# Kernel tuning notes

Hardware: AMD Instinct MI355X
Metric: run time of the kernel (lower is better)

The kernel has to match this reference:

```python
import jax, jax.numpy as jnp
import numpy as np

C = 128
EPS = 1e-5


def _ln(x, g, b):
    m = jnp.mean(x, axis=-1, keepdims=True)
    v = jnp.mean((x - m) ** 2, axis=-1, keepdims=True)
    return (x - m) * jax.lax.rsqrt(v + EPS) * g + b


def setup_inputs() -> dict:
    key = jax.random.key(0)
    ks = jax.random.split(key, 10)
    B, N = 1, 384
    s = 1.0 / np.sqrt(C)
    inp = {
        "z": jax.random.normal(ks[0], (B, N, N, C), dtype=jnp.float32),
        "ln1_g": jnp.ones((C,), jnp.float32),
        "ln1_b": jnp.zeros((C,), jnp.float32),
        "ln2_g": jnp.ones((C,), jnp.float32),
        "ln2_b": jnp.zeros((C,), jnp.float32),
        "Wa": jax.random.uniform(ks[1], (C, C), jnp.float32, -s, s),
        "ba": jnp.zeros((C,), jnp.float32),
        "Wga": jax.random.uniform(ks[2], (C, C), jnp.float32, -s, s),
        "bga": jnp.zeros((C,), jnp.float32),
        "Wb": jax.random.uniform(ks[3], (C, C), jnp.float32, -s, s),
        "bb": jnp.zeros((C,), jnp.float32),
        "Wgb": jax.random.uniform(ks[4], (C, C), jnp.float32, -s, s),
        "bgb": jnp.zeros((C,), jnp.float32),
        "Wg": jax.random.uniform(ks[5], (C, C), jnp.float32, -s, s),
        "bg": jnp.zeros((C,), jnp.float32),
        "Wo": jax.random.uniform(ks[6], (C, C), jnp.float32, -s, s),
        "bo": jnp.zeros((C,), jnp.float32),
    }
    return inp


def reference(z, ln1_g, ln1_b, ln2_g, ln2_b, Wa, ba, Wga, bga, Wb, bb, Wgb, bgb, Wg, bg, Wo, bo):
    # z: (B, i, j, c)
    zn = _ln(z, ln1_g, ln1_b)
    a = (zn @ Wa + ba) * jax.nn.sigmoid(zn @ Wga + bga)      # (B,i,k,c)
    b = (zn @ Wb + bb) * jax.nn.sigmoid(zn @ Wgb + bgb)      # (B,j,k,c)
    gate = jax.nn.sigmoid(zn @ Wg + bg)                      # (B,i,j,c)
    o = jnp.einsum('bikc,bjkc->bijc', a, b)                  # outgoing triangle update
    return gate * (_ln(o, ln2_g, ln2_b) @ Wo + bo)
```

## Files before the change

kernel.cpp:

```cpp
#include <hip/hip_runtime.h>
#include <stdint.h>

typedef _Float16 f16x8 __attribute__((ext_vector_type(8)));
typedef float floatx4 __attribute__((ext_vector_type(4)));

#define RR 147456
#define NC 128
#define NN 384

__device__ inline floatx4 zero4() { floatx4 v; v[0]=0.f; v[1]=0.f; v[2]=0.f; v[3]=0.f; return v; }
__device__ inline float sigmoidf_(float x) { return 1.f / (1.f + __expf(-x)); }

__global__ __launch_bounds__(256) void k0_wt(
    const float* __restrict__ w0, const float* __restrict__ w1,
    const float* __restrict__ w2, const float* __restrict__ w3,
    const float* __restrict__ w4, const float* __restrict__ w5,
    _Float16* __restrict__ wf)
{
  const float* w;
  switch (blockIdx.x) {
    case 0: w = w0; break; case 1: w = w1; break; case 2: w = w2; break;
    case 3: w = w3; break; case 4: w = w4; break; default: w = w5; break;
  }
  _Float16* out = wf + blockIdx.x * 16384;
  const int t = threadIdx.x;
  for (int it = 0; it < 64; ++it) {
    int f = it * 256 + t;
    int j  = f & 7;
    int ln = (f >> 3) & 63;
    int nt = (f >> 9) & 7;
    int k0 = f >> 12;
    int k = k0 * 32 + (ln >> 4) * 8 + j;
    int n = nt * 16 + (ln & 15);
    out[f] = (_Float16)w[k * 128 + n];
  }
}

__global__ __launch_bounds__(256, 4) void k2_ln_gemm(
    const float* __restrict__ z, const float* __restrict__ ln1g, const float* __restrict__ ln1b,
    const _Float16* __restrict__ wf,
    const float* __restrict__ ba, const float* __restrict__ bga,
    const float* __restrict__ bb, const float* __restrict__ bgb,
    const float* __restrict__ bg,
    _Float16* __restrict__ at, _Float16* __restrict__ bt, _Float16* __restrict__ gate)
{
  __shared__ __align__(16) _Float16 zns[64][136];
  __shared__ __align__(16) _Float16 bnc[4][32 * 72];
  const int t = threadIdx.x;
  const int w = t >> 6, lane = t & 63;
  const int l15 = lane & 15, quad = lane >> 4;
  const int r0 = blockIdx.x * 64;
  const int nt0 = w * 2;

  {
    const int g = lane >> 4, h = lane & 15;
    float4 ga = *(const float4*)(ln1g + h*8);
    float4 gb = *(const float4*)(ln1g + h*8 + 4);
    float4 bba = *(const float4*)(ln1b + h*8);
    float4 bbb = *(const float4*)(ln1b + h*8 + 4);
    #pragma unroll
    for (int rr = 0; rr < 4; ++rr) {
      int row = w * 16 + rr * 4 + g;
      const float* zp = z + (size_t)(r0 + row) * NC + h * 8;
      float4 xa = *(const float4*)zp;
      float4 xb = *(const float4*)(zp + 4);
      float s = xa.x + xa.y + xa.z + xa.w + xb.x + xb.y + xb.z + xb.w;
      float q = xa.x*xa.x + xa.y*xa.y + xa.z*xa.z + xa.w*xa.w
              + xb.x*xb.x + xb.y*xb.y + xb.z*xb.z + xb.w*xb.w;
      #pragma unroll
      for (int m = 1; m < 16; m <<= 1) { s += __shfl_xor(s, m); q += __shfl_xor(q, m); }
      float mean = s * (1.f/128.f);
      float var  = q * (1.f/128.f) - mean*mean;
      float rs = rsqrtf(var + 1e-5f);
      union { uint4 u; _Float16 hh[8]; } pk;
      pk.hh[0] = (_Float16)((xa.x - mean) * rs * ga.x + bba.x);
      pk.hh[1] = (_Float16)((xa.y - mean) * rs * ga.y + bba.y);
      pk.hh[2] = (_Float16)((xa.z - mean) * rs * ga.z + bba.z);
      pk.hh[3] = (_Float16)((xa.w - mean) * rs * ga.w + bba.w);
      pk.hh[4] = (_Float16)((xb.x - mean) * rs * gb.x + bbb.x);
      pk.hh[5] = (_Float16)((xb.y - mean) * rs * gb.y + bbb.y);
      pk.hh[6] = (_Float16)((xb.z - mean) * rs * gb.z + bbb.z);
      pk.hh[7] = (_Float16)((xb.w - mean) * rs * gb.w + bbb.w);
      *(uint4*)&zns[row][h * 8] = pk.u;
    }
  }
  __syncthreads();

  const _Float16* pw = wf + lane * 8;
  f16x8 bw[4][2];
  floatx4 acc[4][2];
  union PkU { unsigned int u; _Float16 h[2]; };
  PkU sig[4][2][2];

  auto loadw = [&](int slot) {
    const _Float16* p = pw + slot * 16384;
    #pragma unroll
    for (int k0 = 0; k0 < 4; ++k0)
      #pragma unroll
      for (int j = 0; j < 2; ++j)
        bw[k0][j] = *(const f16x8*)(p + (k0*8 + nt0 + j) * 512);
  };
  auto dogemm = [&]() {
    #pragma unroll
    for (int mt = 0; mt < 4; ++mt) {
      acc[mt][0] = zero4(); acc[mt][1] = zero4();
      #pragma unroll
      for (int k0 = 0; k0 < 4; ++k0) {
        f16x8 af = *(const f16x8*)&zns[mt*16 + l15][k0*32 + quad*8];
        acc[mt][0] = __builtin_amdgcn_mfma_f32_16x16x32_f16(af, bw[k0][0], acc[mt][0], 0, 0, 0);
        acc[mt][1] = __builtin_amdgcn_mfma_f32_16x16x32_f16(af, bw[k0][1], acc[mt][1], 0, 0, 0);
      }
    }
  };
  auto sigpack = [&](const float* big) {
    #pragma unroll
    for (int j = 0; j < 2; ++j) {
      float bgv = big[(nt0 + j)*16 + l15];
      #pragma unroll
      for (int mt = 0; mt < 4; ++mt) {
        sig[mt][j][0].h[0] = (_Float16)sigmoidf_(acc[mt][j][0] + bgv);
        sig[mt][j][0].h[1] = (_Float16)sigmoidf_(acc[mt][j][1] + bgv);
        sig[mt][j][1].h[0] = (_Float16)sigmoidf_(acc[mt][j][2] + bgv);
        sig[mt][j][1].h[1] = (_Float16)sigmoidf_(acc[mt][j][3] + bgv);
      }
    }
  };
  auto bounce_out = [&](_Float16* dst) {
    asm volatile("s_waitcnt lgkmcnt(0)" ::: "memory");
    _Float16* base = dst + (size_t)blockIdx.x * 8192 + w * 2048;
    #pragma unroll
    for (int i = 0; i < 4; ++i) {
      int f = i * 512 + lane * 8;
      int cp = f >> 6, pos = f & 63;
      uint4 v = *(const uint4*)&bnc[w][cp * 72 + pos];
      *(uint4*)(base + f) = v;
    }
  };
  auto combine_store = [&](const float* bia, _Float16* dst) {
    #pragma unroll
    for (int j = 0; j < 2; ++j) {
      int c = (nt0 + j)*16 + l15;
      float bav = bia[c];
      #pragma unroll
      for (int mt = 0; mt < 4; ++mt) {
        union { uint2 u2; _Float16 h[4]; } pk;
        pk.h[0] = (_Float16)((acc[mt][j][0] + bav) * (float)sig[mt][j][0].h[0]);
        pk.h[1] = (_Float16)((acc[mt][j][1] + bav) * (float)sig[mt][j][0].h[1]);
        pk.h[2] = (_Float16)((acc[mt][j][2] + bav) * (float)sig[mt][j][1].h[0]);
        pk.h[3] = (_Float16)((acc[mt][j][3] + bav) * (float)sig[mt][j][1].h[1]);
        *(uint2*)&bnc[w][(j*16 + l15) * 72 + mt*16 + quad*4] = pk.u2;
      }
    }
    bounce_out(dst);
  };

  loadw(1); dogemm(); sigpack(bga);
  loadw(0); dogemm();
  loadw(3);
  combine_store(ba, at);
  dogemm(); sigpack(bgb);
  loadw(2); dogemm();
  loadw(4);
  combine_store(bb, bt);
  dogemm();
  #pragma unroll
  for (int j = 0; j < 2; ++j) {
    float bgv = bg[(nt0 + j)*16 + l15];
    #pragma unroll
    for (int mt = 0; mt < 4; ++mt) {
      union { uint2 u2; _Float16 h[4]; } pk;
      #pragma unroll
      for (int r = 0; r < 4; ++r)
        pk.h[r] = (_Float16)sigmoidf_(acc[mt][j][r] + bgv);
      *(uint2*)&bnc[w][(j*16 + l15) * 72 + mt*16 + quad*4] = pk.u2;
    }
  }
  bounce_out(gate);
}

__global__ __launch_bounds__(256, 3) void k3_tri(
    const _Float16* __restrict__ at, const _Float16* __restrict__ bt, _Float16* __restrict__ o)
{
  __shared__ __align__(16) _Float16 As[2][128 * 40];
  __shared__ __align__(16) _Float16 Bs[2][128 * 40];
  const int t = threadIdx.x;
  const int w = t >> 6, lane = t & 63, l15 = lane & 15, quad = lane >> 4;
  const int c = blockIdx.y;
  const int i0 = (blockIdx.x / 3) * 128, j0 = (blockIdx.x % 3) * 128;
  const int wi = w >> 1, wj = w & 1;

  const int srow = t >> 1, sch = (t & 1) * 16;
  const _Float16* gaRow = at + (size_t)(i0 + srow) * 6 * 8192 + (size_t)c * 64;
  const _Float16* gbRow = bt + (size_t)(j0 + srow) * 6 * 8192 + (size_t)c * 64;
  _Float16* const pa0 = &As[0][srow * 40 + sch];
  _Float16* const pb0 = &Bs[0][srow * 40 + sch];
  _Float16* const pa1 = &As[1][srow * 40 + sch];
  _Float16* const pb1 = &Bs[1][srow * 40 + sch];

  floatx4 acc[4][4];
  #pragma unroll
  for (int mt = 0; mt < 4; ++mt)
    #pragma unroll
    for (int nt = 0; nt < 4; ++nt) acc[mt][nt] = zero4();

  f16x8 aP0,aP1,bP0,bP1, aQ0,aQ1,bQ0,bQ1;

  auto gofs = [&](int kk) -> size_t {
    int x = kk + sch;
    return (size_t)(x >> 6) * 8192 + (size_t)(x & 63);
  };
  auto gloadP = [&](int kk) {
    size_t go = gofs(kk);
    aP0 = *(const f16x8*)(gaRow + go); aP1 = *(const f16x8*)(gaRow + go + 8);
    bP0 = *(const f16x8*)(gbRow + go); bP1 = *(const f16x8*)(gbRow + go + 8);
  };
  auto gloadQ = [&](int kk) {
    size_t go = gofs(kk);
    aQ0 = *(const f16x8*)(gaRow + go); aQ1 = *(const f16x8*)(gaRow + go + 8);
    bQ0 = *(const f16x8*)(gbRow + go); bQ1 = *(const f16x8*)(gbRow + go + 8);
  };
  auto swriteP = [&](int buf) {
    _Float16* pa = buf ? pa1 : pa0; _Float16* pb = buf ? pb1 : pb0;
    *(f16x8*)pa = aP0; *(f16x8*)(pa + 8) = aP1;
    *(f16x8*)pb = bP0; *(f16x8*)(pb + 8) = bP1;
  };
  auto swriteQ = [&](int buf) {
    _Float16* pa = buf ? pa1 : pa0; _Float16* pb = buf ? pb1 : pb0;
    *(f16x8*)pa = aQ0; *(f16x8*)(pa + 8) = aQ1;
    *(f16x8*)pb = bQ0; *(f16x8*)(pb + 8) = bQ1;
  };
  auto compute = [&](int buf) {
    f16x8 af[4], bfr[4];
    #pragma unroll
    for (int mt = 0; mt < 4; ++mt)
      af[mt] = *(const f16x8*)&As[buf][(wi*64 + mt*16 + l15) * 40 + quad*8];
    #pragma unroll
    for (int nt = 0; nt < 4; ++nt)
      bfr[nt] = *(const f16x8*)&Bs[buf][(wj*64 + nt*16 + l15) * 40 + quad*8];
    #pragma unroll
    for (int mt = 0; mt < 4; ++mt)
      #pragma unroll
      for (int nt = 0; nt < 4; ++nt)
        acc[mt][nt] = __builtin_amdgcn_mfma_f32_16x16x32_f16(af[mt], bfr[nt], acc[mt][nt], 0, 0, 0);
  };

  gloadP(0); swriteP(0); gloadP(32);
  __syncthreads();
  #pragma unroll
  for (int s = 0; s < 12; s += 2) {
    if (s + 2 < 12) gloadQ((s + 2) * 32);
    compute(0);
    swriteP(1);
    __syncthreads();
    if (s + 3 < 12) gloadP((s + 3) * 32);
    compute(1);
    if (s + 2 < 12) { swriteQ(0); __syncthreads(); }
  }

  #pragma unroll
  for (int mt = 0; mt < 4; ++mt) {
    #pragma unroll
    for (int r = 0; r < 4; ++r) {
      int i = i0 + wi*64 + mt*16 + quad*4 + r;
      _Float16* obase = o + (size_t)(i*6 + (j0 >> 6) + wj) * 8192 + (size_t)c * 64;
      #pragma unroll
      for (int nt = 0; nt < 4; ++nt) obase[nt*16 + l15] = (_Float16)acc[mt][nt][r];
    }
  }
}

__global__ __launch_bounds__(256, 4) void k4_out(
    const _Float16* __restrict__ o, const _Float16* __restrict__ gate,
    const float* __restrict__ ln2g, const float* __restrict__ ln2b,
    const _Float16* __restrict__ wo5, const float* __restrict__ bo,
    float* __restrict__ out)
{
  __shared__ __align__(16) _Float16 osb[64][136];
  const int t = threadIdx.x;
  const int w = t >> 6, lane = t & 63, l15 = lane & 15, quad = lane >> 4;
  const int r0 = blockIdx.x * 64;
  const int nt0 = w * 2;

  {
    const _Float16* ob = o + (size_t)blockIdx.x * 8192;
    #pragma unroll
    for (int it = 0; it < 4; ++it) {
      int f = (it * 256 + t) * 8;
      int cx = f >> 6, p = f & 63;
      f16x8 v = *(const f16x8*)(ob + f);
      #pragma unroll
      for (int i = 0; i < 8; ++i) osb[p + i][cx] = v[i];
    }
  }
  __syncthreads();

  {
    const int g = lane >> 4, h = lane & 15;
    float4 ga = *(const float4*)(ln2g + h*8);
    float4 gb = *(const float4*)(ln2g + h*8 + 4);
    float4 bba = *(const float4*)(ln2b + h*8);
    float4 bbb = *(const float4*)(ln2b + h*8 + 4);
    #pragma unroll
    for (int rr = 0; rr < 4; ++rr) {
      int row = w * 16 + rr * 4 + g;
      f16x8 xv = *(const f16x8*)&osb[row][h*8];
      float x0 = (float)xv[0], x1 = (float)xv[1], x2 = (float)xv[2], x3 = (float)xv[3];
      float x4 = (float)xv[4], x5 = (float)xv[5], x6 = (float)xv[6], x7 = (float)xv[7];
      float s = x0+x1+x2+x3+x4+x5+x6+x7;
      float q = x0*x0+x1*x1+x2*x2+x3*x3+x4*x4+x5*x5+x6*x6+x7*x7;
      #pragma unroll
      for (int m = 1; m < 16; m <<= 1) { s += __shfl_xor(s, m); q += __shfl_xor(q, m); }
      float mean = s * (1.f/128.f);
      float var  = q * (1.f/128.f) - mean*mean;
      float rs = rsqrtf(var + 1e-5f);
      union { uint4 u; _Float16 hh[8]; } pk;
      pk.hh[0] = (_Float16)((x0 - mean) * rs * ga.x + bba.x);
      pk.hh[1] = (_Float16)((x1 - mean) * rs * ga.y + bba.y);
      pk.hh[2] = (_Float16)((x2 - mean) * rs * ga.z + bba.z);
      pk.hh[3] = (_Float16)((x3 - mean) * rs * ga.w + bba.w);
      pk.hh[4] = (_Float16)((x4 - mean) * rs * gb.x + bbb.x);
      pk.hh[5] = (_Float16)((x5 - mean) * rs * gb.y + bbb.y);
      pk.hh[6] = (_Float16)((x6 - mean) * rs * gb.z + bbb.z);
      pk.hh[7] = (_Float16)((x7 - mean) * rs * gb.w + bbb.w);
      *(uint4*)&osb[row][h * 8] = pk.u;
    }
  }
  __syncthreads();

  f16x8 bw[4][2];
  {
    const _Float16* p = wo5 + lane * 8;
    #pragma unroll
    for (int k0 = 0; k0 < 4; ++k0)
      #pragma unroll
      for (int j = 0; j < 2; ++j)
        bw[k0][j] = *(const f16x8*)(p + (k0*8 + nt0 + j) * 512);
  }
  floatx4 acc[4][2];
  #pragma unroll
  for (int mt = 0; mt < 4; ++mt) {
    acc[mt][0] = zero4(); acc[mt][1] = zero4();
    #pragma unroll
    for (int k0 = 0; k0 < 4; ++k0) {
      f16x8 af = *(const f16x8*)&osb[mt*16 + l15][k0*32 + quad*8];
      acc[mt][0] = __builtin_amdgcn_mfma_f32_16x16x32_f16(af, bw[k0][0], acc[mt][0], 0, 0, 0);
      acc[mt][1] = __builtin_amdgcn_mfma_f32_16x16x32_f16(af, bw[k0][1], acc[mt][1], 0, 0, 0);
    }
  }

  #pragma unroll
  for (int j = 0; j < 2; ++j) {
    int cch = (nt0 + j)*16 + l15;
    float bov = bo[cch];
    #pragma unroll
    for (int mt = 0; mt < 4; ++mt) {
      union { uint2 u2; _Float16 h[4]; } gk;
      gk.u2 = *(const uint2*)(gate + (size_t)blockIdx.x * 8192 + (size_t)cch * 64 + mt*16 + quad*4);
      #pragma unroll
      for (int r = 0; r < 4; ++r) {
        int rl = mt*16 + quad*4 + r;
        out[(size_t)(r0 + rl) * NC + cch] = (float)gk.h[r] * (acc[mt][j][r] + bov);
      }
    }
  }
}

extern "C" void kernel_launch(void* const* d_in, const int* in_sizes, int n_in,
                              void* d_out, int out_size, void* d_ws, size_t ws_size,
                              hipStream_t stream) {
  const float* z    = (const float*)d_in[0];
  const float* l1g  = (const float*)d_in[1];
  const float* l1b  = (const float*)d_in[2];
  const float* l2g  = (const float*)d_in[3];
  const float* l2b  = (const float*)d_in[4];
  const float* Wa   = (const float*)d_in[5];
  const float* ba   = (const float*)d_in[6];
  const float* Wga  = (const float*)d_in[7];
  const float* bga  = (const float*)d_in[8];
  const float* Wb   = (const float*)d_in[9];
  const float* bb   = (const float*)d_in[10];
  const float* Wgb  = (const float*)d_in[11];
  const float* bgb  = (const float*)d_in[12];
  const float* Wg   = (const float*)d_in[13];
  const float* bg   = (const float*)d_in[14];
  const float* Wo   = (const float*)d_in[15];
  const float* bo   = (const float*)d_in[16];

  char* ws = (char*)d_ws;
  _Float16* at_  = (_Float16*)(ws + 0);
  _Float16* bt_  = (_Float16*)(ws + 37748736);
  _Float16* gate = (_Float16*)(ws + 75497472);
  _Float16* o16  = (_Float16*)(ws + 113246208);
  _Float16* wf   = (_Float16*)(ws + 188743680);

  hipLaunchKernelGGL(k0_wt, dim3(6), dim3(256), 0, stream, Wa, Wga, Wb, Wgb, Wg, Wo, wf);
  hipLaunchKernelGGL(k2_ln_gemm, dim3(2304), dim3(256), 0, stream,
                     z, l1g, l1b, wf, ba, bga, bb, bgb, bg, at_, bt_, gate);
  hipLaunchKernelGGL(k3_tri, dim3(9, 128), dim3(256), 0, stream, at_, bt_, o16);
  hipLaunchKernelGGL(k4_out, dim3(2304), dim3(256), 0, stream,
                     o16, gate, l2g, l2b, wf + 5*16384, bo, (float*)d_out);
}
```

Baseline: 323.2 us.

## Use two-wave 64x128 warp tiles in triangle GEMM and nontemporal stores

The triangle-multiply kernel drops from 256 to 128 threads per block. Each wave now computes a 64x128 output tile (4x8 MFMA tiles) instead of 64x64, which raises register-level reuse of the B fragments, and the load/store pipeline is simplified to a single prefetch buffer. Stores of intermediates and the final output become nontemporal to reduce cache pollution. The trade-offs are doubled accumulator register pressure, fewer waves per block to hide latency, and the same LDS footprint per block, so occupancy may drop.

```diff
diff --git a/kernel.cpp b/kernel.cpp
--- a/kernel.cpp
+++ b/kernel.cpp
@@ -3,6 +3,7 @@
 
 typedef _Float16 f16x8 __attribute__((ext_vector_type(8)));
 typedef float floatx4 __attribute__((ext_vector_type(4)));
+typedef unsigned int u32x4 __attribute__((ext_vector_type(4)));
 
 #define RR 147456
 #define NC 128
@@ -132,8 +133,8 @@
     for (int i = 0; i < 4; ++i) {
       int f = i * 512 + lane * 8;
       int cp = f >> 6, pos = f & 63;
-      uint4 v = *(const uint4*)&bnc[w][cp * 72 + pos];
-      *(uint4*)(base + f) = v;
+      u32x4 v = *(const u32x4*)&bnc[w][cp * 72 + pos];
+      __builtin_nontemporal_store(v, (u32x4*)(base + f));
     }
   };
   auto combine_store = [&](const float* bia, _Float16* dst) {
@@ -178,7 +179,7 @@
   bounce_out(gate);
 }
 
-__global__ __launch_bounds__(256, 3) void k3_tri(
+__global__ __launch_bounds__(128, 2) void k3_tri(
     const _Float16* __restrict__ at, const _Float16* __restrict__ bt, _Float16* __restrict__ o)
 {
   __shared__ __align__(16) _Float16 As[2][128 * 40];
@@ -187,84 +188,67 @@
   const int w = t >> 6, lane = t & 63, l15 = lane & 15, quad = lane >> 4;
   const int c = blockIdx.y;
   const int i0 = (blockIdx.x / 3) * 128, j0 = (blockIdx.x % 3) * 128;
-  const int wi = w >> 1, wj = w & 1;
-
-  const int srow = t >> 1, sch = (t & 1) * 16;
-  const _Float16* gaRow = at + (size_t)(i0 + srow) * 6 * 8192 + (size_t)c * 64;
-  const _Float16* gbRow = bt + (size_t)(j0 + srow) * 6 * 8192 + (size_t)c * 64;
-  _Float16* const pa0 = &As[0][srow * 40 + sch];
-  _Float16* const pb0 = &Bs[0][srow * 40 + sch];
-  _Float16* const pa1 = &As[1][srow * 40 + sch];
-  _Float16* const pb1 = &Bs[1][srow * 40 + sch];
-
-  floatx4 acc[4][4];
+
+  const int sj = (t & 3) * 8, sr = t >> 2;
+  f16x8 aS[4], bS[4];
+
+  auto gload = [&](int kk) {
+    size_t ko = ((size_t)(kk >> 6)) * 8192 + (size_t)((kk & 63) + sj) + (size_t)c * 64;
+    #pragma unroll
+    for (int s2 = 0; s2 < 4; ++s2) {
+      int row = s2 * 32 + sr;
+      aS[s2] = *(const f16x8*)(at + (size_t)(i0 + row) * 6 * 8192 + ko);
+      bS[s2] = *(const f16x8*)(bt + (size_t)(j0 + row) * 6 * 8192 + ko);
+    }
+  };
+  auto swrite = [&](int buf) {
+    #pragma unroll
+    for (int s2 = 0; s2 < 4; ++s2) {
+      int row = s2 * 32 + sr;
+      *(f16x8*)&As[buf][row * 40 + sj] = aS[s2];
+      *(f16x8*)&Bs[buf][row * 40 + sj] = bS[s2];
+    }
+  };
+
+  floatx4 acc[4][8];
   #pragma unroll
   for (int mt = 0; mt < 4; ++mt)
     #pragma unroll
-    for (int nt = 0; nt < 4; ++nt) acc[mt][nt] = zero4();
-
-  f16x8 aP0,aP1,bP0,bP1, aQ0,aQ1,bQ0,bQ1;
-
-  auto gofs = [&](int kk) -> size_t {
-    int x = kk + sch;
-    return (size_t)(x >> 6) * 8192 + (size_t)(x & 63);
-  };
-  auto gloadP = [&](int kk) {
-    size_t go = gofs(kk);
-    aP0 = *(const f16x8*)(gaRow + go); aP1 = *(const f16x8*)(gaRow + go + 8);
-    bP0 = *(const f16x8*)(gbRow + go); bP1 = *(const f16x8*)(gbRow + go + 8);
-  };
-  auto gloadQ = [&](int kk) {
-    size_t go = gofs(kk);
-    aQ0 = *(const f16x8*)(gaRow + go); aQ1 = *(const f16x8*)(gaRow + go + 8);
-    bQ0 = *(const f16x8*)(gbRow + go); bQ1 = *(const f16x8*)(gbRow + go + 8);
-  };
-  auto swriteP = [&](int buf) {
-    _Float16* pa = buf ? pa1 : pa0; _Float16* pb = buf ? pb1 : pb0;
-    *(f16x8*)pa = aP0; *(f16x8*)(pa + 8) = aP1;
-    *(f16x8*)pb = bP0; *(f16x8*)(pb + 8) = bP1;
-  };
-  auto swriteQ = [&](int buf) {
-    _Float16* pa = buf ? pa1 : pa0; _Float16* pb = buf ? pb1 : pb0;
-    *(f16x8*)pa = aQ0; *(f16x8*)(pa + 8) = aQ1;
-    *(f16x8*)pb = bQ0; *(f16x8*)(pb + 8) = bQ1;
-  };
+    for (int nt = 0; nt < 8; ++nt) acc[mt][nt] = zero4();
+
   auto compute = [&](int buf) {
-    f16x8 af[4], bfr[4];
+    f16x8 af[4], bfr[8];
     #pragma unroll
     for (int mt = 0; mt < 4; ++mt)
-      af[mt] = *(const f16x8*)&As[buf][(wi*64 + mt*16 + l15) * 40 + quad*8];
-    #pragma unroll
-    for (int nt = 0; nt < 4; ++nt)
-      bfr[nt] = *(const f16x8*)&Bs[buf][(wj*64 + nt*16 + l15) * 40 + quad*8];
+      af[mt] = *(const f16x8*)&As[buf][(w*64 + mt*16 + l15) * 40 + quad*8];
+    #pragma unroll
+    for (int nt = 0; nt < 8; ++nt)
+      bfr[nt] = *(const f16x8*)&Bs[buf][(nt*16 + l15) * 40 + quad*8];
     #pragma unroll
     for (int mt = 0; mt < 4; ++mt)
       #pragma unroll
-      for (int nt = 0; nt < 4; ++nt)
+      for (int nt = 0; nt < 8; ++nt)
         acc[mt][nt] = __builtin_amdgcn_mfma_f32_16x16x32_f16(af[mt], bfr[nt], acc[mt][nt], 0, 0, 0);
   };
 
-  gloadP(0); swriteP(0); gloadP(32);
-  __syncthreads();
-  #pragma unroll
-  for (int s = 0; s < 12; s += 2) {
-    if (s + 2 < 12) gloadQ((s + 2) * 32);
-    compute(0);
-    swriteP(1);
-    __syncthreads();
-    if (s + 3 < 12) gloadP((s + 3) * 32);
-    compute(1);
-    if (s + 2 < 12) { swriteQ(0); __syncthreads(); }
+  gload(0); swrite(0); __syncthreads();
+  for (int s = 0; s < 12; ++s) {
+    if (s + 1 < 12) gload((s + 1) * 32);
+    compute(s & 1);
+    if (s + 1 < 12) { swrite((s + 1) & 1); __syncthreads(); }
   }
 
   #pragma unroll
   for (int mt = 0; mt < 4; ++mt) {
     #pragma unroll
     for (int r = 0; r < 4; ++r) {
-      int i = i0 + wi*64 + mt*16 + quad*4 + r;
-      _Float16* obase = o + (size_t)(i*6 + (j0 >> 6) + wj) * 8192 + (size_t)c * 64;
-      #pragma unroll
-      for (int nt = 0; nt < 4; ++nt) obase[nt*16 + l15] = (_Float16)acc[mt][nt][r];
+      int i = i0 + w*64 + mt*16 + quad*4 + r;
+      _Float16* ob = o + (size_t)(i*6 + (j0 >> 6)) * 8192 + (size_t)c * 64;
+      #pragma unroll
+      for (int nt = 0; nt < 8; ++nt) {
+        _Float16* p = ob + (size_t)(nt >> 2) * 8192 + (nt & 3)*16 + l15;
+        __builtin_nontemporal_store((_Float16)acc[mt][nt][r], p);
+      }
     }
   }
 }
@@ -359,7 +343,8 @@
       #pragma unroll
       for (int r = 0; r < 4; ++r) {
         int rl = mt*16 + quad*4 + r;
-        out[(size_t)(r0 + rl) * NC + cch] = (float)gk.h[r] * (acc[mt][j][r] + bov);
+        __builtin_nontemporal_store((float)gk.h[r] * (acc[mt][j][r] + bov),
+                                    out + (size_t)(r0 + rl) * NC + cch);
       }
     }
   }
@@ -396,7 +381,7 @@
   hipLaunchKernelGGL(k0_wt, dim3(6), dim3(256), 0, stream, Wa, Wga, Wb, Wgb, Wg, Wo, wf);
   hipLaunchKernelGGL(k2_ln_gemm, dim3(2304), dim3(256), 0, stream,
                      z, l1g, l1b, wf, ba, bga, bb, bgb, bg, at_, bt_, gate);
-  hipLaunchKernelGGL(k3_tri, dim3(9, 128), dim3(256), 0, stream, at_, bt_, o16);
+  hipLaunchKernelGGL(k3_tri, dim3(9, 128), dim3(128), 0, stream, at_, bt_, o16);
   hipLaunchKernelGGL(k4_out, dim3(2304), dim3(256), 0, stream,
                      o16, gate, l2g, l2b, wf + 5*16384, bo, (float*)d_out);
 }
```

Result: slower. 335.9 us (+3.9%).

## Double-buffer projection weights, prefetch gate/weights early, use nontemporal stores

Applied to the files above, without the earlier changes.

The projection kernel now keeps two weight register buffers, so the next weight slice loads while the current GEMM runs. The output kernel issues its weight and gate loads before the LN stage to hide their latency. Stores of the intermediate at/bt/gate tensors, the triangle output and the final output become nontemporal, to reduce cache pollution. This raises register pressure, which may hurt occupancy, and nontemporal stores of data read right afterwards could miss in L2.

```diff
diff --git a/kernel.cpp b/kernel.cpp
--- a/kernel.cpp
+++ b/kernel.cpp
@@ -3,6 +3,7 @@
 
 typedef _Float16 f16x8 __attribute__((ext_vector_type(8)));
 typedef float floatx4 __attribute__((ext_vector_type(4)));
+typedef unsigned int u32x4 __attribute__((ext_vector_type(4)));
 
 #define RR 147456
 #define NC 128
@@ -87,12 +88,12 @@
   __syncthreads();
 
   const _Float16* pw = wf + lane * 8;
-  f16x8 bw[4][2];
+  f16x8 bwA[4][2], bwB[4][2];
   floatx4 acc[4][2];
   union PkU { unsigned int u; _Float16 h[2]; };
   PkU sig[4][2][2];
 
-  auto loadw = [&](int slot) {
+  auto loadw = [&](f16x8 (&bw)[4][2], int slot) {
     const _Float16* p = pw + slot * 16384;
     #pragma unroll
     for (int k0 = 0; k0 < 4; ++k0)
@@ -100,7 +101,7 @@
       for (int j = 0; j < 2; ++j)
         bw[k0][j] = *(const f16x8*)(p + (k0*8 + nt0 + j) * 512);
   };
-  auto dogemm = [&]() {
+  auto dogemm = [&](const f16x8 (&bw)[4][2]) {
     #pragma unroll
     for (int mt = 0; mt < 4; ++mt) {
       acc[mt][0] = zero4(); acc[mt][1] = zero4();
@@ -132,8 +133,8 @@
     for (int i = 0; i < 4; ++i) {
       int f = i * 512 + lane * 8;
       int cp = f >> 6, pos = f & 63;
-      uint4 v = *(const uint4*)&bnc[w][cp * 72 + pos];
-      *(uint4*)(base + f) = v;
+      u32x4 v = *(const u32x4*)&bnc[w][cp * 72 + pos];
+      __builtin_nontemporal_store(v, (u32x4*)(base + f));
     }
   };
   auto combine_store = [&](const float* bia, _Float16* dst) {
@@ -154,15 +155,15 @@
     bounce_out(dst);
   };
 
-  loadw(1); dogemm(); sigpack(bga);
-  loadw(0); dogemm();
-  loadw(3);
-  combine_store(ba, at);
-  dogemm(); sigpack(bgb);
-  loadw(2); dogemm();
-  loadw(4);
-  combine_store(bb, bt);
-  dogemm();
+  loadw(bwA, 1); loadw(bwB, 0);
+  dogemm(bwA); sigpack(bga);
+  loadw(bwA, 3);
+  dogemm(bwB); combine_store(ba, at);
+  loadw(bwB, 2);
+  dogemm(bwA); sigpack(bgb);
+  loadw(bwA, 4);
+  dogemm(bwB); combine_store(bb, bt);
+  dogemm(bwA);
   #pragma unroll
   for (int j = 0; j < 2; ++j) {
     float bgv = bg[(nt0 + j)*16 + l15];
@@ -264,7 +265,8 @@
       int i = i0 + wi*64 + mt*16 + quad*4 + r;
       _Float16* obase = o + (size_t)(i*6 + (j0 >> 6) + wj) * 8192 + (size_t)c * 64;
       #pragma unroll
-      for (int nt = 0; nt < 4; ++nt) obase[nt*16 + l15] = (_Float16)acc[mt][nt][r];
+      for (int nt = 0; nt < 4; ++nt)
+        __builtin_nontemporal_store((_Float16)acc[mt][nt][r], obase + nt*16 + l15);
     }
   }
 }
@@ -280,6 +282,25 @@
   const int w = t >> 6, lane = t & 63, l15 = lane & 15, quad = lane >> 4;
   const int r0 = blockIdx.x * 64;
   const int nt0 = w * 2;
+
+  f16x8 bw[4][2];
+  {
+    const _Float16* p = wo5 + lane * 8;
+    #pragma unroll
+    for (int k0 = 0; k0 < 4; ++k0)
+      #pragma unroll
+      for (int j = 0; j < 2; ++j)
+        bw[k0][j] = *(const f16x8*)(p + (k0*8 + nt0 + j) * 512);
+  }
+  union GkU { uint2 u2; _Float16 h[4]; };
+  GkU gk[2][4];
+  #pragma unroll
+  for (int j = 0; j < 2; ++j) {
+    int cch = (nt0 + j)*16 + l15;
+    #pragma unroll
+    for (int mt = 0; mt < 4; ++mt)
+      gk[j][mt].u2 = *(const uint2*)(gate + (size_t)blockIdx.x * 8192 + (size_t)cch * 64 + mt*16 + quad*4);
+  }
 
   {
     const _Float16* ob = o + (size_t)blockIdx.x * 8192;
@@ -327,15 +348,6 @@
   }
   __syncthreads();
 
-  f16x8 bw[4][2];
-  {
-    const _Float16* p = wo5 + lane * 8;
-    #pragma unroll
-    for (int k0 = 0; k0 < 4; ++k0)
-      #pragma unroll
-      for (int j = 0; j < 2; ++j)
-        bw[k0][j] = *(const f16x8*)(p + (k0*8 + nt0 + j) * 512);
-  }
   floatx4 acc[4][2];
   #pragma unroll
   for (int mt = 0; mt < 4; ++mt) {
@@ -354,12 +366,11 @@
     float bov = bo[cch];
     #pragma unroll
     for (int mt = 0; mt < 4; ++mt) {
-      union { uint2 u2; _Float16 h[4]; } gk;
-      gk.u2 = *(const uint2*)(gate + (size_t)blockIdx.x * 8192 + (size_t)cch * 64 + mt*16 + quad*4);
       #pragma unroll
       for (int r = 0; r < 4; ++r) {
         int rl = mt*16 + quad*4 + r;
-        out[(size_t)(r0 + rl) * NC + cch] = (float)gk.h[r] * (acc[mt][j][r] + bov);
+        __builtin_nontemporal_store((float)gk[j][mt].h[r] * (acc[mt][j][r] + bov),
+                                    out + (size_t)(r0 + rl) * NC + cch);
       }
     }
   }
```

After: 342.8 us. +6.1%, slower.
